# Kernel tuning notes

Hardware: AMD Instinct MI355X
Metric: run time of the kernel (lower is better)

## Reference

```python
import jax, jax.numpy as jnp
import numpy as np

D_MODEL = 1024
N_HEADS = 16
D_HEAD = D_MODEL // N_HEADS
B, T = 4, 2048


def setup_inputs() -> dict:
    key = jax.random.key(0)
    ks = jax.random.split(key, 9)
    s = 0.02
    return {
        "x": jax.random.normal(ks[0], (B, T, D_MODEL), dtype=jnp.float32),
        "Wq": jax.random.normal(ks[1], (D_MODEL, D_MODEL), dtype=jnp.float32) * s,
        "bq": jnp.zeros((D_MODEL,), dtype=jnp.float32),
        "Wk": jax.random.normal(ks[2], (D_MODEL, D_MODEL), dtype=jnp.float32) * s,
        "bk": jnp.zeros((D_MODEL,), dtype=jnp.float32),
        "Wv": jax.random.normal(ks[3], (D_MODEL, D_MODEL), dtype=jnp.float32) * s,
        "bv": jnp.zeros((D_MODEL,), dtype=jnp.float32),
        "Wo": jax.random.normal(ks[4], (D_MODEL, D_MODEL), dtype=jnp.float32) * s,
        "bo": jnp.zeros((D_MODEL,), dtype=jnp.float32),
    }


def reference(x, Wq, bq, Wk, bk, Wv, bv, Wo, bo):
    # Dropout in eval mode (identity), as standard for a correctness baseline.
    Bx, Tx, _ = x.shape
    # torch nn.Linear: y = x @ W.T + b
    Q = x @ Wq.T + bq
    K = x @ Wk.T + bk
    V = x @ Wv.T + bv
    # [B, T, H, Dh] -> [B, H, T, Dh]
    Q = Q.reshape(Bx, Tx, N_HEADS, D_HEAD).transpose(0, 2, 1, 3)
    K = K.reshape(Bx, Tx, N_HEADS, D_HEAD).transpose(0, 2, 1, 3)
    V = V.reshape(Bx, Tx, N_HEADS, D_HEAD).transpose(0, 2, 1, 3)
    scale = 1.0 / jnp.sqrt(jnp.float32(D_HEAD))
    scores = jnp.einsum("bhqd,bhkd->bhqk", Q, K) * scale  # [B,H,T,T]
    # additive causal mask: -1e6 above the diagonal (matches torch.triu trick)
    mask = jnp.triu(jnp.full((Tx, Tx), -1000000.0, dtype=scores.dtype), k=1)
    scores = scores + mask
    attn = jax.nn.softmax(scores, axis=-1)
    out = jnp.einsum("bhqk,bhkd->bhqd", attn, V)  # [B,H,T,Dh]
    out = out.transpose(0, 2, 1, 3).reshape(Bx, Tx, D_MODEL)
    out = out @ Wo.T + bo
    return out
```

## Files before the change

### kernel.cpp

```cpp
#include <hip/hip_runtime.h>
#include <stdint.h>

#define DM 1024
#define HEADS 16
#define DH 64
#define BQ 4
#define TT 2048
#define MTOT (BQ*TT)
#define NQT (TT/64)

typedef __attribute__((ext_vector_type(8))) __bf16 bf16x8;
typedef __attribute__((ext_vector_type(4))) float f32x4;
typedef __attribute__((ext_vector_type(4))) uint32_t u32x4;
typedef unsigned short u16;
typedef __attribute__((ext_vector_type(8))) unsigned short u16x8;

__device__ __forceinline__ u16 f2b(float f) {
  uint32_t u = __builtin_bit_cast(uint32_t, f);
  u = (u + 0x7fffu + ((u >> 16) & 1u)) >> 16;
  return (u16)u;
}

__device__ __forceinline__ uint32_t cvtpk(float lo, float hi) {
  uint32_t r;
  asm("v_cvt_pk_bf16_f32 %0, %1, %2" : "=v"(r) : "v"(lo), "v"(hi));
  return r;
}

__device__ __forceinline__ void gload_lds16(const u16* g, u16* l) {
  __builtin_amdgcn_global_load_lds(
      (const __attribute__((address_space(1))) void*)g,
      (__attribute__((address_space(3))) void*)l, 16, 0, 0);
}

#define NX (MTOT * DM / 4)
#define NW (DM * DM / 4)
__global__ __launch_bounds__(256) void cast_all(const float* __restrict__ x,
                                                const float* __restrict__ Wq,
                                                const float* __restrict__ Wk,
                                                const float* __restrict__ Wv,
                                                const float* __restrict__ Wo,
                                                u16* __restrict__ xb,
                                                u16* __restrict__ wqkvb,
                                                u16* __restrict__ wob) {
  int i = blockIdx.x * 256 + threadIdx.x;
  const float* src; u16* dst;
  if (i < NX)               { src = x;  dst = xb; }
  else if (i < NX + NW)     { src = Wq; dst = wqkvb;          i -= NX; }
  else if (i < NX + 2 * NW) { src = Wk; dst = wqkvb + 4 * NW; i -= NX + NW; }
  else if (i < NX + 3 * NW) { src = Wv; dst = wqkvb + 8 * NW; i -= NX + 2 * NW; }
  else                      { src = Wo; dst = wob;            i -= NX + 3 * NW; }
  float4 v = ((const float4*)src)[i];
  ushort4 o;
  o.x = f2b(v.x); o.y = f2b(v.y); o.z = f2b(v.z); o.w = f2b(v.w);
  ((ushort4*)dst)[i] = o;
}

#define BKq 32
#define NKq (DM / BKq)
#define SLOT_A (256 * BKq)
#define SLOT_E (2 * SLOT_A)

__global__ __launch_bounds__(512, 2) void gemm_qkv8(const u16* __restrict__ A,
                                                    const u16* __restrict__ W,
                                                    const float* __restrict__ bq,
                                                    const float* __restrict__ bk,
                                                    const float* __restrict__ bv,
                                                    u16* __restrict__ Qo,
                                                    u16* __restrict__ Ko,
                                                    u16* __restrict__ Vto,
                                                    float qs) {
  __shared__ u16 lds[4 * SLOT_E];
  const int tid = threadIdx.x, lane = tid & 63, wave = tid >> 6;
  const int fr = lane & 15, g = lane >> 4;
  const int wm = wave >> 2, wn = wave & 3;

  int bid = blockIdx.x;
  bid = (bid & 7) * 48 + (bid >> 3);
  const int bx = bid % 12, by = bid / 12;
  const int m0 = by * 256, n0 = bx * 256;

  const int srow = tid >> 2;
  const int schunk = (tid & 3) ^ ((tid >> 3) & 3);
  const u16* gA0 = A + (size_t)(m0 + srow) * DM + schunk * 8;
  const u16* gA1 = gA0 + (size_t)128 * DM;
  const u16* gB0 = W + (size_t)(n0 + srow) * DM + schunk * 8;
  const u16* gB1 = gB0 + (size_t)128 * DM;
  const int dA0 = wave * 512;
  const int dA1 = 4096 + wave * 512;
  const int dB0 = SLOT_A + wave * 512;
  const int dB1 = SLOT_A + 4096 + wave * 512;

#define STAGE_Ah(slot, kt) {                                 \
    u16* ls = &lds[(slot) * SLOT_E];                         \
    const int ke = (kt) * BKq;                               \
    gload_lds16(gA0 + ke, ls + dA0);                         \
    gload_lds16(gA1 + ke, ls + dA1); }
#define STAGE_Bh(slot, kt) {                                 \
    u16* ls = &lds[(slot) * SLOT_E];                         \
    const int ke = (kt) * BKq;                               \
    gload_lds16(gB0 + ke, ls + dB0);                         \
    gload_lds16(gB1 + ke, ls + dB1); }

  const int rchunk = (g ^ ((fr >> 1) & 3)) * 8;
  const int offA = (wm * 128 + fr) * 32 + rchunk;
  const int offB = SLOT_A + (wn * 64 + fr) * 32 + rchunk;

  f32x4 acc[8][4];
#pragma unroll
  for (int mi = 0; mi < 8; ++mi)
#pragma unroll
    for (int ni = 0; ni < 4; ++ni) acc[mi][ni] = (f32x4){0.f, 0.f, 0.f, 0.f};

  bf16x8 afA[8], bfA[4], afB[8], bfB[4];

#define READ_P1(AFv, BFv, kt) {                              \
    const u16* sl = &lds[((kt) & 3) * SLOT_E];               \
    _Pragma("unroll")                                        \
    for (int mi = 0; mi < 4; ++mi)                           \
      AFv[mi] = *(const bf16x8*)&sl[offA + mi * 512];        \
    _Pragma("unroll")                                        \
    for (int ni = 0; ni < 4; ++ni)                           \
      BFv[ni] = *(const bf16x8*)&sl[offB + ni * 512]; }
#define READ_P2(AFv, kt) {                                   \
    const u16* sl = &lds[((kt) & 3) * SLOT_E];               \
    _Pragma("unroll")                                        \
    for (int mi = 4; mi < 8; ++mi)                           \
      AFv[mi] = *(const bf16x8*)&sl[offA + mi * 512]; }

#define MFMA_P1(AFv, BFv) {                                  \
    __builtin_amdgcn_s_setprio(1);                           \
    _Pragma("unroll")                                        \
    for (int mi = 0; mi < 4; ++mi)                           \
      _Pragma("unroll")                                      \
      for (int ni = 0; ni < 4; ++ni)                         \
        acc[mi][ni] = __builtin_amdgcn_mfma_f32_16x16x32_bf16(AFv[mi], BFv[ni], acc[mi][ni], 0, 0, 0); \
    __builtin_amdgcn_s_setprio(0); }
#define MFMA_P2(AFv, BFv) {                                  \
    __builtin_amdgcn_s_setprio(1);                           \
    _Pragma("unroll")                                        \
    for (int mi = 4; mi < 8; ++mi)                           \
      _Pragma("unroll")                                      \
      for (int ni = 0; ni < 4; ++ni)                         \
        acc[mi][ni] = __builtin_amdgcn_mfma_f32_16x16x32_bf16(AFv[mi], BFv[ni], acc[mi][ni], 0, 0, 0); \
    __builtin_amdgcn_s_setprio(0); }

#define BARQ asm volatile("s_barrier" ::: "memory");
#define WAIT4 asm volatile("s_waitcnt vmcnt(4)" ::: "memory"); BARQ
#define WAIT0 asm volatile("s_waitcnt vmcnt(0)" ::: "memory"); BARQ

#define STEP(AFc, BFc, AFn, BFn, kt, DO_STAGE) {             \
    WAIT4                                                    \
    READ_P1(AFn, BFn, (kt) + 1)                              \
    MFMA_P1(AFc, BFc)                                        \
    if (DO_STAGE) STAGE_Ah(((kt) + 3) & 3, (kt) + 3)         \
    BARQ                                                     \
    READ_P2(AFn, (kt) + 1)                                   \
    MFMA_P2(AFc, BFc)                                        \
    if (DO_STAGE) STAGE_Bh(((kt) + 3) & 3, (kt) + 3) }

  STAGE_Ah(0, 0) STAGE_Bh(0, 0)
  STAGE_Ah(1, 1) STAGE_Bh(1, 1)
  STAGE_Ah(2, 2) STAGE_Bh(2, 2)
  asm volatile("s_waitcnt vmcnt(8)" ::: "memory");
  asm volatile("s_barrier" ::: "memory");
  READ_P1(afA, bfA, 0)
  READ_P2(afA, 0)

  for (int kt = 0; kt < NKq - 4; kt += 2) {
    STEP(afA, bfA, afB, bfB, kt, true)
    STEP(afB, bfB, afA, bfA, kt + 1, true)
  }
  STEP(afA, bfA, afB, bfB, NKq - 4, true)
  STEP(afB, bfB, afA, bfA, NKq - 3, false)
  WAIT0
  READ_P1(afB, bfB, NKq - 1)
  MFMA_P1(afA, bfA)
  BARQ
  READ_P2(afB, NKq - 1)
  MFMA_P2(afA, bfA)
  MFMA_P1(afB, bfB)
  MFMA_P2(afB, bfB)

  const int g4 = g * 4;
  const int seg = n0 >> 10;
  const int nbase = (n0 & 1023) + wn * 64 + fr;
  if (seg == 0) {
#pragma unroll
    for (int ni = 0; ni < 4; ++ni) {
      const int cgl = nbase + ni * 16;
      const float bb = bq[cgl];
      const int hh = cgl >> 6, d = cgl & 63;
#pragma unroll
      for (int mi = 0; mi < 8; ++mi) {
        const int m = m0 + wm * 128 + mi * 16 + g4;
        const int bi = m >> 11, t = m & 2047;
        u16* dst = &Qo[(((size_t)bi * HEADS + hh) * TT + t) * DH + d];
#pragma unroll
        for (int j = 0; j < 4; ++j)
          dst[(size_t)j * DH] = f2b((acc[mi][ni][j] + bb) * qs);
      }
    }
  } else if (seg == 1) {
#pragma unroll
    for (int ni = 0; ni < 4; ++ni) {
      const int cgl = nbase + ni * 16;
      const float bb = bk[cgl];
      const int hh = cgl >> 6, d = cgl & 63;
#pragma unroll
      for (int mi = 0; mi < 8; ++mi) {
        const int m = m0 + wm * 128 + mi * 16 + g4;
        const int bi = m >> 11, t = m & 2047;
        u16* dst = &Ko[(((size_t)bi * HEADS + hh) * TT + t) * DH + d];
#pragma unroll
        for (int j = 0; j < 4; ++j)
          dst[(size_t)j * DH] = f2b(acc[mi][ni][j] + bb);
      }
    }
  } else {
#pragma unroll
    for (int ni = 0; ni < 4; ++ni) {
      const int cgl = nbase + ni * 16;
      const float bb = bv[cgl];
      const int hh = cgl >> 6, d = cgl & 63;
#pragma unroll
      for (int mi = 0; mi < 8; ++mi) {
        const int t0 = (m0 + wm * 128 + mi * 16 + g4) & 2047;
        const int bi = (m0 + wm * 128 + mi * 16 + g4) >> 11;
        const int w64 = t0 & 63;
        const int pos = (t0 & ~63) | (((w64 >> 5) & 1) << 5) | (((w64 >> 2) & 3) << 3) |
                        (((w64 >> 4) & 1) << 2);
        ushort4 o;
        o.x = f2b(acc[mi][ni][0] + bb);
        o.y = f2b(acc[mi][ni][1] + bb);
        o.z = f2b(acc[mi][ni][2] + bb);
        o.w = f2b(acc[mi][ni][3] + bb);
        *(ushort4*)&Vto[(((size_t)bi * HEADS + hh) * DH + d) * TT + pos] = o;
      }
    }
  }
#undef STAGE_Ah
#undef STAGE_Bh
#undef READ_P1
#undef READ_P2
#undef MFMA_P1
#undef MFMA_P2
#undef STEP
#undef BARQ
#undef WAIT4
#undef WAIT0
}

#define SLOT_OA (256 * 32)
#define SLOT_OB (128 * 32)
#define SLOT_OE (SLOT_OA + SLOT_OB)

__global__ __launch_bounds__(512, 2) void gemm_out8(const u16* __restrict__ A,
                                                    const u16* __restrict__ Bw,
                                                    const float* __restrict__ bias,
                                                    float* __restrict__ outp) {
  __shared__ u16 lds[4 * SLOT_OE];
  const int tid = threadIdx.x, lane = tid & 63, wave = tid >> 6;
  const int fr = lane & 15, g = lane >> 4;
  const int wm = wave >> 1, wn = wave & 1;

  const int bx = blockIdx.x >> 5, by = blockIdx.x & 31;
  const int m0 = by * 256, n0 = bx * 128;

  const int srow = tid >> 2;
  const int schunk = (tid & 3) ^ ((tid >> 3) & 3);
  const u16* gA0 = A + (size_t)(m0 + srow) * DM + schunk * 8;
  const u16* gA1 = gA0 + (size_t)128 * DM;
  const u16* gB0 = Bw + (size_t)(n0 + srow) * DM + schunk * 8;
  const int dA0 = wave * 512;
  const int dA1 = 4096 + wave * 512;
  const int dB0 = SLOT_OA + wave * 512;

#define STAGEO(slot, kt) {                                   \
    u16* ls = &lds[(slot) * SLOT_OE];                        \
    const int ke = (kt) * 32;                                \
    gload_lds16(gA0 + ke, ls + dA0);                         \
    gload_lds16(gA1 + ke, ls + dA1);                         \
    gload_lds16(gB0 + ke, ls + dB0); }

  const int rchunk = (g ^ ((fr >> 1) & 3)) * 8;
  const int offA = (wm * 64 + fr) * 32 + rchunk;
  const int offB = SLOT_OA + (wn * 64 + fr) * 32 + rchunk;

  f32x4 acc[4][4];
#pragma unroll
  for (int mi = 0; mi < 4; ++mi)
#pragma unroll
    for (int ni = 0; ni < 4; ++ni) acc[mi][ni] = (f32x4){0.f, 0.f, 0.f, 0.f};

  bf16x8 afA[4], bfA[4], afB[4], bfB[4];

#define READO(AFv, BFv, kt) {                                \
    const u16* sl = &lds[((kt) & 3) * SLOT_OE];              \
    _Pragma("unroll")                                        \
    for (int mi = 0; mi < 4; ++mi)                           \
      AFv[mi] = *(const bf16x8*)&sl[offA + mi * 512];        \
    _Pragma("unroll")                                        \
    for (int ni = 0; ni < 4; ++ni)                           \
      BFv[ni] = *(const bf16x8*)&sl[offB + ni * 512]; }

#define MFMAO(AFv, BFv) {                                    \
    __builtin_amdgcn_s_setprio(1);                           \
    _Pragma("unroll")                                        \
    for (int mi = 0; mi < 4; ++mi)                           \
      _Pragma("unroll")                                      \
      for (int ni = 0; ni < 4; ++ni)                         \
        acc[mi][ni] = __builtin_amdgcn_mfma_f32_16x16x32_bf16(AFv[mi], BFv[ni], acc[mi][ni], 0, 0, 0); \
    __builtin_amdgcn_s_setprio(0); }

#define OW3 asm volatile("s_waitcnt vmcnt(3)" ::: "memory"); \
            asm volatile("s_barrier" ::: "memory");
#define OW0 asm volatile("s_waitcnt vmcnt(0)" ::: "memory"); \
            asm volatile("s_barrier" ::: "memory");

  STAGEO(0, 0)
  STAGEO(1, 1)
  STAGEO(2, 2)
  asm volatile("s_waitcnt vmcnt(6)" ::: "memory");
  asm volatile("s_barrier" ::: "memory");
  READO(afA, bfA, 0)

  for (int kt = 0; kt < 28; kt += 2) {
    OW3
    READO(afB, bfB, kt + 1)
    MFMAO(afA, bfA)
    STAGEO((kt + 3) & 3, kt + 3)
    OW3
    READO(afA, bfA, kt + 2)
    MFMAO(afB, bfB)
    STAGEO((kt + 4) & 3, kt + 4)
  }
  OW3
  READO(afB, bfB, 29)
  MFMAO(afA, bfA)
  STAGEO(3, 31)
  OW3
  READO(afA, bfA, 30)
  MFMAO(afB, bfB)
  OW0
  READO(afB, bfB, 31)
  MFMAO(afA, bfA)
  MFMAO(afB, bfB)

  const int g4 = g * 4;
#pragma unroll
  for (int mi = 0; mi < 4; ++mi) {
    const int rg = m0 + wm * 64 + mi * 16 + g4;
#pragma unroll
    for (int ni = 0; ni < 4; ++ni) {
      const int cg = n0 + wn * 64 + ni * 16 + fr;
      const float bb = bias[cg];
#pragma unroll
      for (int j = 0; j < 4; ++j)
        outp[(size_t)(rg + j) * DM + cg] = acc[mi][ni][j] + bb;
    }
  }
#undef STAGEO
#undef READO
#undef MFMAO
#undef OW3
#undef OW0
}

__global__ __launch_bounds__(256) void attn_fwd(const u16* __restrict__ Q,
                                                const u16* __restrict__ K,
                                                const u16* __restrict__ Vt,
                                                u16* __restrict__ O) {
  const int o_ = blockIdx.x;
  const int r_ = o_ & 7, q_ = o_ >> 3;
  const int gidx = r_ * 8 + (q_ >> 4);
  const int pj = q_ & 15;
  const int b = gidx >> 4, h = gidx & 15;
  const int tid = threadIdx.x, lane = tid & 63, wave = tid >> 6;
  __shared__ u16 Ks[64 * 64];
  __shared__ u16 Vs[64 * 64];

  const size_t bh = ((size_t)b * HEADS + h) * TT;
  const size_t vbse = ((size_t)b * HEADS + h) * DH;
  const int fr = lane & 15, g = lane >> 4;
  const int sr = tid >> 2;
  const int sc0 = tid & 3;

  const int sw1 = (sc0 ^ (sr & 7)) * 8;
  const int sw2 = ((sc0 + 4) ^ (sr & 7)) * 8;
  const int sgc = sc0 * 8;
  const int rk0 = (g ^ (fr & 7)) * 8;
  const int rk1 = ((4 + g) ^ (fr & 7)) * 8;

  for (int pass = 0; pass < 2; ++pass) {
    const int qt = pass ? pj : (NQT - 1 - pj);
    const int q0 = qt * 64;
    const int qrow = q0 + wave * 16 + fr;
    const int k8 = g * 8;
    const bf16x8 qf0 = *(const bf16x8*)&Q[(bh + qrow) * DH + k8];
    const bf16x8 qf1 = *(const bf16x8*)&Q[(bh + qrow) * DH + 32 + k8];

    float lsum = 0.f;
    f32x4 oacc[4];
#pragma unroll
    for (int c = 0; c < 4; ++c) oacc[c] = (f32x4){0.f, 0.f, 0.f, 0.f};

    for (int kvb = 0; kvb <= qt; ++kvb) {
      const int kv0 = kvb * 64;
      {
        const u16* kg = &K[(bh + kv0 + sr) * DH + sgc];
        u16x8 ka = *(const u16x8*)kg;
        u16x8 kc = *(const u16x8*)(kg + 32);
        const u16* vg = &Vt[(vbse + sr) * TT + kv0 + sgc];
        u16x8 va = *(const u16x8*)vg;
        u16x8 vc = *(const u16x8*)(vg + 32);
        *(u16x8*)&Ks[sr * 64 + sw1] = ka;
        *(u16x8*)&Ks[sr * 64 + sw2] = kc;
        *(u16x8*)&Vs[sr * 64 + sw1] = va;
        *(u16x8*)&Vs[sr * 64 + sw2] = vc;
      }
      __syncthreads();

      f32x4 s[4];
      __builtin_amdgcn_s_setprio(1);
#pragma unroll
      for (int c = 0; c < 4; ++c) {
        bf16x8 kb0 = *(const bf16x8*)&Ks[(c * 16 + fr) * 64 + rk0];
        bf16x8 kb1 = *(const bf16x8*)&Ks[(c * 16 + fr) * 64 + rk1];
        f32x4 t = (f32x4){0.f, 0.f, 0.f, 0.f};
        t = __builtin_amdgcn_mfma_f32_16x16x32_bf16(kb0, qf0, t, 0, 0, 0);
        t = __builtin_amdgcn_mfma_f32_16x16x32_bf16(kb1, qf1, t, 0, 0, 0);
        s[c] = t;
      }
      __builtin_amdgcn_s_setprio(0);

      if (kvb == qt) {
#pragma unroll
        for (int c = 0; c < 4; ++c) {
          const int colg = kv0 + c * 16 + 4 * g;
#pragma unroll
          for (int r = 0; r < 4; ++r)
            if (colg + r > qrow) s[c][r] = -1e30f;
        }
      }

      float rs = 0.f;
      uint32_t pk[8];
#pragma unroll
      for (int c = 0; c < 4; ++c) {
        float p0 = __builtin_amdgcn_exp2f(s[c][0]);
        float p1 = __builtin_amdgcn_exp2f(s[c][1]);
        float p2 = __builtin_amdgcn_exp2f(s[c][2]);
        float p3 = __builtin_amdgcn_exp2f(s[c][3]);
        rs += (p0 + p1) + (p2 + p3);
        pk[2 * c] = cvtpk(p0, p1);
        pk[2 * c + 1] = cvtpk(p2, p3);
      }
      rs += __shfl_xor(rs, 16);
      rs += __shfl_xor(rs, 32);
      lsum += rs;

      const bf16x8 pa0 = __builtin_bit_cast(bf16x8, (u32x4){pk[0], pk[1], pk[2], pk[3]});
      const bf16x8 pa1 = __builtin_bit_cast(bf16x8, (u32x4){pk[4], pk[5], pk[6], pk[7]});

      __builtin_amdgcn_s_setprio(1);
#pragma unroll
      for (int c = 0; c < 4; ++c) {
        bf16x8 vb0 = *(const bf16x8*)&Vs[(c * 16 + fr) * 64 + rk0];
        bf16x8 vb1 = *(const bf16x8*)&Vs[(c * 16 + fr) * 64 + rk1];
        oacc[c] = __builtin_amdgcn_mfma_f32_16x16x32_bf16(vb0, pa0, oacc[c], 0, 0, 0);
        oacc[c] = __builtin_amdgcn_mfma_f32_16x16x32_bf16(vb1, pa1, oacc[c], 0, 0, 0);
      }
      __builtin_amdgcn_s_setprio(0);
      __syncthreads();
    }

    const float inv = 1.f / lsum;
#pragma unroll
    for (int c = 0; c < 4; ++c) {
      ushort4 o;
      o.x = f2b(oacc[c][0] * inv);
      o.y = f2b(oacc[c][1] * inv);
      o.z = f2b(oacc[c][2] * inv);
      o.w = f2b(oacc[c][3] * inv);
      *(ushort4*)&O[((size_t)b * TT + qrow) * DM + h * DH + c * 16 + 4 * g] = o;
    }
  }
}

extern "C" void kernel_launch(void* const* d_in, const int* in_sizes, int n_in,
                              void* d_out, int out_size, void* d_ws, size_t ws_size,
                              hipStream_t stream) {
  const float* x  = (const float*)d_in[0];
  const float* Wq = (const float*)d_in[1];
  const float* bq = (const float*)d_in[2];
  const float* Wk = (const float*)d_in[3];
  const float* bk = (const float*)d_in[4];
  const float* Wv = (const float*)d_in[5];
  const float* bv = (const float*)d_in[6];
  const float* Wo = (const float*)d_in[7];
  const float* bo = (const float*)d_in[8];

  char* w = (char*)d_ws;
  u16* xb    = (u16*)w; w += (size_t)MTOT * DM * 2;
  u16* Wqkvb = (u16*)w; w += (size_t)3 * DM * DM * 2;
  u16* Wob   = (u16*)w; w += (size_t)DM * DM * 2;
  u16* Qb    = (u16*)w; w += (size_t)MTOT * DM * 2;
  u16* Kb    = (u16*)w; w += (size_t)MTOT * DM * 2;
  u16* Vtb   = (u16*)w; w += (size_t)MTOT * DM * 2;
  u16* AOb   = (u16*)w; w += (size_t)MTOT * DM * 2;

  cast_all<<<(NX + 4 * NW) / 256, 256, 0, stream>>>(x, Wq, Wk, Wv, Wo, xb, Wqkvb, Wob);

  const float qs = 0.125f * 1.44269504f;
  gemm_qkv8<<<384, 512, 0, stream>>>(xb, Wqkvb, bq, bk, bv, Qb, Kb, Vtb, qs);

  attn_fwd<<<1024, 256, 0, stream>>>(Qb, Kb, Vtb, AOb);

  gemm_out8<<<256, 512, 0, stream>>>(AOb, Wob, bo, (float*)d_out);
}
```

Measured before the change: 161.0 us.

## Process paired causal query tiles jointly to share K/V staging

The attention kernel previously ran two sequential passes over KV blocks, one per paired query tile (a long one and a short one). It now loads both query tiles up front and walks the shared KV prefix once, computing scores and PV products for both tiles from the same LDS-staged K/V block. It then continues with only the long tile for the remaining blocks. This removes the redundant global loads, LDS stores and barriers for the overlapping KV range. The cost is roughly doubled accumulator and score registers in the joint loop, which may reduce occupancy.

```diff
diff --git a/kernel.cpp b/kernel.cpp
--- a/kernel.cpp
+++ b/kernel.cpp
@@ -391,101 +391,194 @@
   const int sgc = sc0 * 8;
   const int rk0 = (g ^ (fr & 7)) * 8;
   const int rk1 = ((4 + g) ^ (fr & 7)) * 8;
-
-  for (int pass = 0; pass < 2; ++pass) {
-    const int qt = pass ? pj : (NQT - 1 - pj);
-    const int q0 = qt * 64;
-    const int qrow = q0 + wave * 16 + fr;
-    const int k8 = g * 8;
-    const bf16x8 qf0 = *(const bf16x8*)&Q[(bh + qrow) * DH + k8];
-    const bf16x8 qf1 = *(const bf16x8*)&Q[(bh + qrow) * DH + 32 + k8];
-
-    float lsum = 0.f;
-    f32x4 oacc[4];
-#pragma unroll
-    for (int c = 0; c < 4; ++c) oacc[c] = (f32x4){0.f, 0.f, 0.f, 0.f};
-
-    for (int kvb = 0; kvb <= qt; ++kvb) {
-      const int kv0 = kvb * 64;
-      {
-        const u16* kg = &K[(bh + kv0 + sr) * DH + sgc];
-        u16x8 ka = *(const u16x8*)kg;
-        u16x8 kc = *(const u16x8*)(kg + 32);
-        const u16* vg = &Vt[(vbse + sr) * TT + kv0 + sgc];
-        u16x8 va = *(const u16x8*)vg;
-        u16x8 vc = *(const u16x8*)(vg + 32);
-        *(u16x8*)&Ks[sr * 64 + sw1] = ka;
-        *(u16x8*)&Ks[sr * 64 + sw2] = kc;
-        *(u16x8*)&Vs[sr * 64 + sw1] = va;
-        *(u16x8*)&Vs[sr * 64 + sw2] = vc;
+  const int k8 = g * 8;
+
+  const int qtA = NQT - 1 - pj, qtB = pj;
+  const int qrowA = qtA * 64 + wave * 16 + fr;
+  const int qrowB = qtB * 64 + wave * 16 + fr;
+  const bf16x8 qfA0 = *(const bf16x8*)&Q[(bh + qrowA) * DH + k8];
+  const bf16x8 qfA1 = *(const bf16x8*)&Q[(bh + qrowA) * DH + 32 + k8];
+  const bf16x8 qfB0 = *(const bf16x8*)&Q[(bh + qrowB) * DH + k8];
+  const bf16x8 qfB1 = *(const bf16x8*)&Q[(bh + qrowB) * DH + 32 + k8];
+
+  float lsumA = 0.f, lsumB = 0.f;
+  f32x4 oaccA[4], oaccB[4];
+#pragma unroll
+  for (int c = 0; c < 4; ++c) {
+    oaccA[c] = (f32x4){0.f, 0.f, 0.f, 0.f};
+    oaccB[c] = (f32x4){0.f, 0.f, 0.f, 0.f};
+  }
+
+#define STAGE_KV(kv0) {                                          \
+    const u16* kg = &K[(bh + (kv0) + sr) * DH + sgc];            \
+    u16x8 ka = *(const u16x8*)kg;                                \
+    u16x8 kc = *(const u16x8*)(kg + 32);                         \
+    const u16* vg = &Vt[(vbse + sr) * TT + (kv0) + sgc];         \
+    u16x8 va = *(const u16x8*)vg;                                \
+    u16x8 vc = *(const u16x8*)(vg + 32);                         \
+    *(u16x8*)&Ks[sr * 64 + sw1] = ka;                            \
+    *(u16x8*)&Ks[sr * 64 + sw2] = kc;                            \
+    *(u16x8*)&Vs[sr * 64 + sw1] = va;                            \
+    *(u16x8*)&Vs[sr * 64 + sw2] = vc;                            \
+  }
+
+  for (int kvb = 0; kvb <= qtB; ++kvb) {
+    const int kv0 = kvb * 64;
+    STAGE_KV(kv0)
+    __syncthreads();
+
+    f32x4 sA[4], sB[4];
+    __builtin_amdgcn_s_setprio(1);
+#pragma unroll
+    for (int c = 0; c < 4; ++c) {
+      bf16x8 kb0 = *(const bf16x8*)&Ks[(c * 16 + fr) * 64 + rk0];
+      bf16x8 kb1 = *(const bf16x8*)&Ks[(c * 16 + fr) * 64 + rk1];
+      f32x4 tA = (f32x4){0.f, 0.f, 0.f, 0.f};
+      tA = __builtin_amdgcn_mfma_f32_16x16x32_bf16(kb0, qfA0, tA, 0, 0, 0);
+      tA = __builtin_amdgcn_mfma_f32_16x16x32_bf16(kb1, qfA1, tA, 0, 0, 0);
+      sA[c] = tA;
+      f32x4 tB = (f32x4){0.f, 0.f, 0.f, 0.f};
+      tB = __builtin_amdgcn_mfma_f32_16x16x32_bf16(kb0, qfB0, tB, 0, 0, 0);
+      tB = __builtin_amdgcn_mfma_f32_16x16x32_bf16(kb1, qfB1, tB, 0, 0, 0);
+      sB[c] = tB;
+    }
+    __builtin_amdgcn_s_setprio(0);
+
+    if (kvb == qtB) {
+#pragma unroll
+      for (int c = 0; c < 4; ++c) {
+        const int colg = kv0 + c * 16 + 4 * g;
+#pragma unroll
+        for (int r = 0; r < 4; ++r)
+          if (colg + r > qrowB) sB[c][r] = -1e30f;
       }
-      __syncthreads();
-
-      f32x4 s[4];
-      __builtin_amdgcn_s_setprio(1);
+    }
+
+    float rsA = 0.f, rsB = 0.f;
+    uint32_t pkA[8], pkB[8];
+#pragma unroll
+    for (int c = 0; c < 4; ++c) {
+      float a0 = __builtin_amdgcn_exp2f(sA[c][0]);
+      float a1 = __builtin_amdgcn_exp2f(sA[c][1]);
+      float a2 = __builtin_amdgcn_exp2f(sA[c][2]);
+      float a3 = __builtin_amdgcn_exp2f(sA[c][3]);
+      rsA += (a0 + a1) + (a2 + a3);
+      pkA[2 * c] = cvtpk(a0, a1);
+      pkA[2 * c + 1] = cvtpk(a2, a3);
+      float b0 = __builtin_amdgcn_exp2f(sB[c][0]);
+      float b1 = __builtin_amdgcn_exp2f(sB[c][1]);
+      float b2 = __builtin_amdgcn_exp2f(sB[c][2]);
+      float b3 = __builtin_amdgcn_exp2f(sB[c][3]);
+      rsB += (b0 + b1) + (b2 + b3);
+      pkB[2 * c] = cvtpk(b0, b1);
+      pkB[2 * c + 1] = cvtpk(b2, b3);
+    }
+    rsA += __shfl_xor(rsA, 16);
+    rsA += __shfl_xor(rsA, 32);
+    lsumA += rsA;
+    rsB += __shfl_xor(rsB, 16);
+    rsB += __shfl_xor(rsB, 32);
+    lsumB += rsB;
+
+    const bf16x8 paA0 = __builtin_bit_cast(bf16x8, (u32x4){pkA[0], pkA[1], pkA[2], pkA[3]});
+    const bf16x8 paA1 = __builtin_bit_cast(bf16x8, (u32x4){pkA[4], pkA[5], pkA[6], pkA[7]});
+    const bf16x8 paB0 = __builtin_bit_cast(bf16x8, (u32x4){pkB[0], pkB[1], pkB[2], pkB[3]});
+    const bf16x8 paB1 = __builtin_bit_cast(bf16x8, (u32x4){pkB[4], pkB[5], pkB[6], pkB[7]});
+
+    __builtin_amdgcn_s_setprio(1);
+#pragma unroll
+    for (int c = 0; c < 4; ++c) {
+      bf16x8 vb0 = *(const bf16x8*)&Vs[(c * 16 + fr) * 64 + rk0];
+      bf16x8 vb1 = *(const bf16x8*)&Vs[(c * 16 + fr) * 64 + rk1];
+      oaccA[c] = __builtin_amdgcn_mfma_f32_16x16x32_bf16(vb0, paA0, oaccA[c], 0, 0, 0);
+      oaccA[c] = __builtin_amdgcn_mfma_f32_16x16x32_bf16(vb1, paA1, oaccA[c], 0, 0, 0);
+      oaccB[c] = __builtin_amdgcn_mfma_f32_16x16x32_bf16(vb0, paB0, oaccB[c], 0, 0, 0);
+      oaccB[c] = __builtin_amdgcn_mfma_f32_16x16x32_bf16(vb1, paB1, oaccB[c], 0, 0, 0);
+    }
+    __builtin_amdgcn_s_setprio(0);
+    __syncthreads();
+  }
+
+  for (int kvb = qtB + 1; kvb <= qtA; ++kvb) {
+    const int kv0 = kvb * 64;
+    STAGE_KV(kv0)
+    __syncthreads();
+
+    f32x4 sA[4];
+    __builtin_amdgcn_s_setprio(1);
+#pragma unroll
+    for (int c = 0; c < 4; ++c) {
+      bf16x8 kb0 = *(const bf16x8*)&Ks[(c * 16 + fr) * 64 + rk0];
+      bf16x8 kb1 = *(const bf16x8*)&Ks[(c * 16 + fr) * 64 + rk1];
+      f32x4 tA = (f32x4){0.f, 0.f, 0.f, 0.f};
+      tA = __builtin_amdgcn_mfma_f32_16x16x32_bf16(kb0, qfA0, tA, 0, 0, 0);
+      tA = __builtin_amdgcn_mfma_f32_16x16x32_bf16(kb1, qfA1, tA, 0, 0, 0);
+      sA[c] = tA;
+    }
+    __builtin_amdgcn_s_setprio(0);
+
+    if (kvb == qtA) {
 #pragma unroll
       for (int c = 0; c < 4; ++c) {
-        bf16x8 kb0 = *(const bf16x8*)&Ks[(c * 16 + fr) * 64 + rk0];
-        bf16x8 kb1 = *(const bf16x8*)&Ks[(c * 16 + fr) * 64 + rk1];
-        f32x4 t = (f32x4){0.f, 0.f, 0.f, 0.f};
-        t = __builtin_amdgcn_mfma_f32_16x16x32_bf16(kb0, qf0, t, 0, 0, 0);
-        t = __builtin_amdgcn_mfma_f32_16x16x32_bf16(kb1, qf1, t, 0, 0, 0);
-        s[c] = t;
+        const int colg = kv0 + c * 16 + 4 * g;
+#pragma unroll
+        for (int r = 0; r < 4; ++r)
+          if (colg + r > qrowA) sA[c][r] = -1e30f;
       }
-      __builtin_amdgcn_s_setprio(0);
-
-      if (kvb == qt) {
-#pragma unroll
-        for (int c = 0; c < 4; ++c) {
-          const int colg = kv0 + c * 16 + 4 * g;
-#pragma unroll
-          for (int r = 0; r < 4; ++r)
-            if (colg + r > qrow) s[c][r] = -1e30f;
-        }
-      }
-
-      float rs = 0.f;
-      uint32_t pk[8];
-#pragma unroll
-      for (int c = 0; c < 4; ++c) {
-        float p0 = __builtin_amdgcn_exp2f(s[c][0]);
-        float p1 = __builtin_amdgcn_exp2f(s[c][1]);
-        float p2 = __builtin_amdgcn_exp2f(s[c][2]);
-        float p3 = __builtin_amdgcn_exp2f(s[c][3]);
-        rs += (p0 + p1) + (p2 + p3);
-        pk[2 * c] = cvtpk(p0, p1);
-        pk[2 * c + 1] = cvtpk(p2, p3);
-      }
-      rs += __shfl_xor(rs, 16);
-      rs += __shfl_xor(rs, 32);
-      lsum += rs;
-
-      const bf16x8 pa0 = __builtin_bit_cast(bf16x8, (u32x4){pk[0], pk[1], pk[2], pk[3]});
-      const bf16x8 pa1 = __builtin_bit_cast(bf16x8, (u32x4){pk[4], pk[5], pk[6], pk[7]});
-
-      __builtin_amdgcn_s_setprio(1);
-#pragma unroll
-      for (int c = 0; c < 4; ++c) {
-        bf16x8 vb0 = *(const bf16x8*)&Vs[(c * 16 + fr) * 64 + rk0];
-        bf16x8 vb1 = *(const bf16x8*)&Vs[(c * 16 + fr) * 64 + rk1];
-        oacc[c] = __builtin_amdgcn_mfma_f32_16x16x32_bf16(vb0, pa0, oacc[c], 0, 0, 0);
-        oacc[c] = __builtin_amdgcn_mfma_f32_16x16x32_bf16(vb1, pa1, oacc[c], 0, 0, 0);
-      }
-      __builtin_amdgcn_s_setprio(0);
-      __syncthreads();
-    }
-
-    const float inv = 1.f / lsum;
+    }
+
+    float rsA = 0.f;
+    uint32_t pkA[8];
 #pragma unroll
     for (int c = 0; c < 4; ++c) {
-      ushort4 o;
-      o.x = f2b(oacc[c][0] * inv);
-      o.y = f2b(oacc[c][1] * inv);
-      o.z = f2b(oacc[c][2] * inv);
-      o.w = f2b(oacc[c][3] * inv);
-      *(ushort4*)&O[((size_t)b * TT + qrow) * DM + h * DH + c * 16 + 4 * g] = o;
-    }
-  }
+      float a0 = __builtin_amdgcn_exp2f(sA[c][0]);
+      float a1 = __builtin_amdgcn_exp2f(sA[c][1]);
+      float a2 = __builtin_amdgcn_exp2f(sA[c][2]);
+      float a3 = __builtin_amdgcn_exp2f(sA[c][3]);
+      rsA += (a0 + a1) + (a2 + a3);
+      pkA[2 * c] = cvtpk(a0, a1);
+      pkA[2 * c + 1] = cvtpk(a2, a3);
+    }
+    rsA += __shfl_xor(rsA, 16);
+    rsA += __shfl_xor(rsA, 32);
+    lsumA += rsA;
+
+    const bf16x8 paA0 = __builtin_bit_cast(bf16x8, (u32x4){pkA[0], pkA[1], pkA[2], pkA[3]});
+    const bf16x8 paA1 = __builtin_bit_cast(bf16x8, (u32x4){pkA[4], pkA[5], pkA[6], pkA[7]});
+
+    __builtin_amdgcn_s_setprio(1);
+#pragma unroll
+    for (int c = 0; c < 4; ++c) {
+      bf16x8 vb0 = *(const bf16x8*)&Vs[(c * 16 + fr) * 64 + rk0];
+      bf16x8 vb1 = *(const bf16x8*)&Vs[(c * 16 + fr) * 64 + rk1];
+      oaccA[c] = __builtin_amdgcn_mfma_f32_16x16x32_bf16(vb0, paA0, oaccA[c], 0, 0, 0);
+      oaccA[c] = __builtin_amdgcn_mfma_f32_16x16x32_bf16(vb1, paA1, oaccA[c], 0, 0, 0);
+    }
+    __builtin_amdgcn_s_setprio(0);
+    __syncthreads();
+  }
+
+  const float invA = 1.f / lsumA;
+#pragma unroll
+  for (int c = 0; c < 4; ++c) {
+    ushort4 o;
+    o.x = f2b(oaccA[c][0] * invA);
+    o.y = f2b(oaccA[c][1] * invA);
+    o.z = f2b(oaccA[c][2] * invA);
+    o.w = f2b(oaccA[c][3] * invA);
+    *(ushort4*)&O[((size_t)b * TT + qrowA) * DM + h * DH + c * 16 + 4 * g] = o;
+  }
+  const float invB = 1.f / lsumB;
+#pragma unroll
+  for (int c = 0; c < 4; ++c) {
+    ushort4 o;
+    o.x = f2b(oaccB[c][0] * invB);
+    o.y = f2b(oaccB[c][1] * invB);
+    o.z = f2b(oaccB[c][2] * invB);
+    o.w = f2b(oaccB[c][3] * invB);
+    *(ushort4*)&O[((size_t)b * TT + qrowB) * DM + h * DH + c * 16 + 4 * g] = o;
+  }
+#undef STAGE_KV
 }
 
 extern "C" void kernel_launch(void* const* d_in, const int* in_sizes, int n_in,
```

Measured after the change: 174.4 us. 1.08x slower.
